# Optimization experiments

Hardware: AMD Instinct MI355X
Metric: run time of the kernel (lower is better)

The kernel has to match this reference:

```python
import jax, jax.numpy as jnp
import numpy as np
import math

SEQ_LEN = 2048
DIM = 4096
N_HEADS = 32
N_KV_HEADS = 8
HEAD_DIM = DIM // N_HEADS  # 128
ROPE_THETA = 500000.0
W_SCALE = 0.02


def _precompute_freqs(head_dim, end, theta=ROPE_THETA):
    freq = 1.0 / theta ** (jnp.arange(0, head_dim, 2, dtype=jnp.float32) / head_dim)  # [hd/2]
    t = jnp.arange(end, dtype=jnp.float32)
    f = t[:, None] * freq[None, :]  # [S, hd/2]
    return jnp.cos(f), jnp.sin(f)


def _apply_rope(x, cos, sin):
    # x: [S, H, hd]; interleaved even/odd rotation, matching torch ::2 / 1::2 indexing
    xe = x[:, :, 0::2]
    xo = x[:, :, 1::2]
    c = cos[:, None, :]  # [S, 1, hd/2]
    s = sin[:, None, :]
    re = xe * c - xo * s
    ro = xe * s + xo * c
    # re-interleave: out[..., 2i] = re[..., i], out[..., 2i+1] = ro[..., i]
    return jnp.stack([re, ro], axis=-1).reshape(x.shape)


def setup_inputs() -> dict:
    key = jax.random.key(0)
    k = jax.random.split(key, 5)
    x = jax.random.normal(k[0], (SEQ_LEN, DIM), dtype=jnp.float32)
    wq = jax.random.normal(k[1], (DIM, DIM), dtype=jnp.float32) * W_SCALE
    wk = jax.random.normal(k[2], (N_KV_HEADS * HEAD_DIM, DIM), dtype=jnp.float32) * W_SCALE
    wv = jax.random.normal(k[3], (N_KV_HEADS * HEAD_DIM, DIM), dtype=jnp.float32) * W_SCALE
    wo = jax.random.normal(k[4], (DIM, DIM), dtype=jnp.float32) * W_SCALE
    return {"x": x, "wq": wq, "wk": wk, "wv": wv, "wo": wo}


def reference(x, wq, wk, wv, wo):
    S = SEQ_LEN
    rep = N_HEADS // N_KV_HEADS  # 4

    Q = (x @ wq.T).reshape(S, N_HEADS, HEAD_DIM)
    K = (x @ wk.T).reshape(S, N_KV_HEADS, HEAD_DIM)
    V = (x @ wv.T).reshape(S, N_KV_HEADS, HEAD_DIM)

    cos, sin = _precompute_freqs(HEAD_DIM, S)
    Q = _apply_rope(Q, cos, sin)
    K = _apply_rope(K, cos, sin)

    # GQA: repeat_interleave(K, rep, dim=1) maps query head h -> kv group h // rep.
    # Express natively with a grouped einsum instead of materializing repeated K/V.
    Qg = Q.transpose(1, 0, 2).reshape(N_KV_HEADS, rep, S, HEAD_DIM)  # [g, r, S, d]
    Kt = K.transpose(1, 0, 2)  # [g, S, d]
    Vt = V.transpose(1, 0, 2)  # [g, S, d]

    scores = jnp.einsum('grqd,gkd->grqk', Qg, Kt) / math.sqrt(HEAD_DIM)
    mask = jnp.triu(jnp.full((S, S), -jnp.inf, dtype=scores.dtype), k=1)
    probs = jax.nn.softmax(scores + mask, axis=-1)
    out = jnp.einsum('grqk,gkd->grqd', probs, Vt)  # [g, r, S, d]

    out = out.reshape(N_HEADS, S, HEAD_DIM).transpose(1, 0, 2).reshape(S, N_HEADS * HEAD_DIM)
    return out @ wo.T
```

## Files before the change

### kernel.cpp

```cpp
#include <hip/hip_runtime.h>

typedef unsigned short u16;
typedef short short8 __attribute__((ext_vector_type(8)));
typedef float f32x4 __attribute__((ext_vector_type(4)));
typedef unsigned short u16x4 __attribute__((ext_vector_type(4)));

typedef short8 short8_a __attribute__((may_alias));
typedef f32x4 f32x4_a __attribute__((may_alias));
typedef u16x4 u16x4_a __attribute__((may_alias));
typedef unsigned int uint_a __attribute__((may_alias));

__device__ __forceinline__ u16 f2b(float f) {
  unsigned u = __float_as_uint(f);
  u += 0x7FFFu + ((u >> 16) & 1u);
  return (u16)(u >> 16);
}

__device__ __forceinline__ void mfma_b(f32x4& d, short8 a, short8 b) {
  asm("v_mfma_f32_16x16x32_bf16 %0, %1, %2, %0" : "+v"(d) : "v"(a), "v"(b));
}

__device__ __forceinline__ void guard4(f32x4& a, f32x4& b, f32x4& c, f32x4& d) {
  asm volatile("s_nop 7\n\ts_nop 7" : "+v"(a), "+v"(b), "+v"(c), "+v"(d));
}
__device__ __forceinline__ void guard8(f32x4* o) {
  asm volatile("s_nop 7\n\ts_nop 7"
               : "+v"(o[0]), "+v"(o[1]), "+v"(o[2]), "+v"(o[3]),
                 "+v"(o[4]), "+v"(o[5]), "+v"(o[6]), "+v"(o[7]));
}

__device__ __forceinline__ void gload16(const void* g, void* l) {
  __builtin_amdgcn_global_load_lds((__attribute__((address_space(1))) void*)(g),
                                   (__attribute__((address_space(3))) void*)(l),
                                   16, 0, 0);
}

__device__ __forceinline__ void bar_v4() {
  asm volatile("s_waitcnt vmcnt(4)\n\ts_barrier" ::: "memory");
}
__device__ __forceinline__ void bar_v0() {
  asm volatile("s_waitcnt vmcnt(0)\n\ts_barrier" ::: "memory");
}

__global__ __launch_bounds__(256)
void k_prep(const float* __restrict__ x, const float* __restrict__ wq,
            const float* __restrict__ wk, const float* __restrict__ wv,
            const float* __restrict__ wo, u16* __restrict__ xb,
            u16* __restrict__ wB, u16* __restrict__ wob,
            float* __restrict__ cost, float* __restrict__ sint) {
  const long i = (long)blockIdx.x * 256 + threadIdx.x;
  const float* src;
  u16* dst;
  long j;
  if (i < 6291456) {
    if (i < 2097152) { src = x; dst = xb; j = i; }
    else { src = wq; dst = wB; j = i - 2097152; }
  } else if (i < 8388608) {
    if (i < 7340032) { src = wk; dst = wB + 16777216; j = i - 6291456; }
    else { src = wv; dst = wB + 20971520; j = i - 7340032; }
  } else if (i < 12582912) {
    src = wo; dst = wob; j = i - 8388608;
  } else {
    long ti = i - 12582912;
    int s = (int)(ti >> 6), jj = (int)(ti & 63);
    float freq = powf(500000.0f, -(float)jj * (1.0f / 64.0f));
    float a = (float)s * freq;
    float sv, cv;
    sincosf(a, &sv, &cv);
    cost[ti] = cv;
    sint[ti] = sv;
    return;
  }
  f32x4 v = ((const f32x4_a*)src)[j];
  u16x4 o;
  o[0] = f2b(v[0]); o[1] = f2b(v[1]); o[2] = f2b(v[2]); o[3] = f2b(v[3]);
  ((u16x4_a*)dst)[j] = o;
}

#define QK_SCALE 0.08838834764831845f
template <int EPI>
__global__ __launch_bounds__(256, 2)
void k_gemm_t(const u16* __restrict__ A, const u16* __restrict__ B,
              float* __restrict__ C, int M, int N, int K,
              const float* __restrict__ cost, const float* __restrict__ sint,
              u16* __restrict__ Qb, u16* __restrict__ Kb, u16* __restrict__ Vt) {
  __shared__ u16 As[12288];
  __shared__ u16 Bs[12288];
  const int tid = threadIdx.x;
  const int w = tid >> 6, lane = tid & 63;
  const int hi = lane >> 4, lo = lane & 15;
  const int nwg = gridDim.x;
  int bid = blockIdx.x;
  if ((nwg & 7) == 0) bid = (bid & 7) * (nwg >> 3) + (bid >> 3);
  const int ntn = N >> 7;
  const int tm = bid / ntn, tn = bid - tm * ntn;
  const int m0 = tm << 7, n0 = tn << 7;
  const int wr = w >> 1, wc = w & 1;

  const int rowl = w * 16 + (lane >> 2);
  const int ks = (((lane & 3) ^ ((lane >> 3) & 3)) << 3);
  const u16* Ag0 = A + (long)(m0 + rowl) * K + ks;
  const u16* Ag1 = A + (long)(m0 + 64 + rowl) * K + ks;
  const u16* Bg0 = B + (long)(n0 + rowl) * K + ks;
  const u16* Bg1 = B + (long)(n0 + 64 + rowl) * K + ks;
  const int sb = w * 512;

  f32x4 acc[4][4] = {};
  const int hs = hi ^ ((lo >> 1) & 3);
  const int aoff = (wr * 64 + lo) * 32 + hs * 8;
  const int boff = (wc * 64 + lo) * 32 + hs * 8;

  const int nt = K >> 5;
  int c0 = 0, c1 = 4096, c2 = 8192;

  gload16(Ag0, As + c0 + sb);       gload16(Ag1, As + c0 + sb + 2048);
  gload16(Bg0, Bs + c0 + sb);       gload16(Bg1, Bs + c0 + sb + 2048);
  gload16(Ag0 + 32, As + c1 + sb);  gload16(Ag1 + 32, As + c1 + sb + 2048);
  gload16(Bg0 + 32, Bs + c1 + sb);  gload16(Bg1 + 32, Bs + c1 + sb + 2048);
  bar_v4();

  for (int t = 0; t < nt; ++t) {
    if (t + 2 < nt) {
      const int k0 = (t + 2) << 5;
      gload16(Ag0 + k0, As + c2 + sb);
      gload16(Ag1 + k0, As + c2 + sb + 2048);
      gload16(Bg0 + k0, Bs + c2 + sb);
      gload16(Bg1 + k0, Bs + c2 + sb + 2048);
    }
    short8 af[4], bf[4];
#pragma unroll
    for (int m = 0; m < 4; ++m)
      af[m] = *(const short8_a*)(As + c0 + aoff + m * 512);
#pragma unroll
    for (int n = 0; n < 4; ++n)
      bf[n] = *(const short8_a*)(Bs + c0 + boff + n * 512);
    __builtin_amdgcn_s_setprio(1);
#pragma unroll
    for (int m = 0; m < 4; ++m)
#pragma unroll
      for (int n = 0; n < 4; ++n) mfma_b(acc[m][n], af[m], bf[n]);
    __builtin_amdgcn_s_setprio(0);
    if (t + 2 < nt) bar_v4();
    else bar_v0();
    const int tmp = c0; c0 = c1; c1 = c2; c2 = tmp;
  }
  guard8(&acc[0][0]);
  guard8(&acc[2][0]);

  if constexpr (EPI == 0) {
#pragma unroll
    for (int m = 0; m < 4; ++m) {
      const int row0 = m0 + wr * 64 + m * 16 + hi * 4;
#pragma unroll
      for (int n = 0; n < 4; ++n) {
        const int col = n0 + wc * 64 + n * 16 + lo;
#pragma unroll
        for (int r = 0; r < 4; ++r)
          C[(long)(row0 + r) * N + col] = acc[m][n][r];
      }
    }
  } else {
    if (n0 < 5120) {
      const bool isQ = (n0 < 4096);
#pragma unroll
      for (int m = 0; m < 4; ++m) {
        const int row0 = m0 + wr * 64 + m * 16 + hi * 4;
#pragma unroll
        for (int n = 0; n < 4; ++n) {
          const int c = n0 + wc * 64 + n * 16 + lo;
          const int j0 = (c & 127) >> 1;
          const bool even = ((c & 1) == 0);
#pragma unroll
          for (int r = 0; r < 4; ++r) {
            float own = acc[m][n][r];
            float part = __shfl_xor(own, 1);
            const int s_ = row0 + r;
            const float cv = cost[s_ * 64 + j0];
            const float sv = sint[s_ * 64 + j0];
            float res = even ? (own * cv - part * sv) : (part * sv + own * cv);
            if (isQ)
              Qb[(long)s_ * 4096 + c] = f2b(res * QK_SCALE);
            else
              Kb[(long)s_ * 1024 + (c - 4096)] = f2b(res);
          }
        }
      }
    } else {
#pragma unroll
      for (int m = 0; m < 4; ++m) {
        const int row0 = m0 + wr * 64 + m * 16 + hi * 4;
#pragma unroll
        for (int n = 0; n < 4; ++n) {
          const int vc = n0 - 5120 + wc * 64 + n * 16 + lo;
          u16x4 pk;
#pragma unroll
          for (int r = 0; r < 4; ++r) pk[r] = f2b(acc[m][n][r]);
          *(u16x4_a*)(Vt + (long)vc * 2048 + row0) = pk;
        }
      }
    }
  }
}

#define KLD 136
#define VLD 72
__global__ __launch_bounds__(256, 2)
void k_attn(const u16* __restrict__ Qb, const u16* __restrict__ Kb,
            const u16* __restrict__ Vt, u16* __restrict__ Ab) {
  __shared__ u16 Ks[64 * KLD];
  __shared__ u16 Vs[128 * VLD];
  __shared__ u16 Ps[4 * 16 * VLD];

  const int tid = threadIdx.x;
  const int w = tid >> 6, lane = tid & 63;
  const int hi = lane >> 4, lo = lane & 15;
  const int qt = 31 - (blockIdx.x >> 5);
  const int h = blockIdx.x & 31;
  const int hkv = h >> 2;
  const int q0 = qt * 64;
  const int qrow = q0 + w * 16 + lo;

  short8 qf[4];
#pragma unroll
  for (int c = 0; c < 4; ++c)
    qf[c] = *(const short8_a*)(Qb + (long)qrow * 4096 + h * 128 + c * 32 + hi * 8);

  f32x4 o[8] = {};
  float m_run = -1e30f, l_run = 0.f;
  u16* Pw = Ps + w * (16 * VLD);

  const int ntiles = qt + 1;
  for (int t = 0; t < ntiles; ++t) {
    const int kv0 = t * 64;
    __syncthreads();
#pragma unroll
    for (int r = 0; r < 4; ++r) {
      int i = r * 256 + tid;
      int key = i >> 4, d8 = (i & 15) * 8;
      short8 v = *(const short8_a*)(Kb + (long)(kv0 + key) * 1024 + hkv * 128 + d8);
      *(short8_a*)(Ks + key * KLD + d8) = v;
    }
#pragma unroll
    for (int r = 0; r < 4; ++r) {
      int i = r * 256 + tid;
      int dd = i >> 3, k8 = (i & 7) * 8;
      short8 v = *(const short8_a*)(Vt + (long)hkv * 262144 + (long)dd * 2048 + kv0 + k8);
      *(short8_a*)(Vs + dd * VLD + k8) = v;
    }
    __syncthreads();

    f32x4 sc[4] = {};
#pragma unroll
    for (int c = 0; c < 4; ++c) {
#pragma unroll
      for (int kt = 0; kt < 4; ++kt) {
        short8 kf = *(const short8_a*)(Ks + (kt * 16 + lo) * KLD + c * 32 + hi * 8);
        mfma_b(sc[kt], kf, qf[c]);
      }
    }
    guard4(sc[0], sc[1], sc[2], sc[3]);

    if (t == ntiles - 1) {
#pragma unroll
      for (int kt = 0; kt < 4; ++kt)
#pragma unroll
        for (int r = 0; r < 4; ++r) {
          int key = kv0 + kt * 16 + hi * 4 + r;
          if (key > qrow) sc[kt][r] = -1e30f;
        }
    }
    float tmax = -1e30f;
#pragma unroll
    for (int kt = 0; kt < 4; ++kt)
#pragma unroll
      for (int r = 0; r < 4; ++r) tmax = fmaxf(tmax, sc[kt][r]);
    tmax = fmaxf(tmax, __shfl_xor(tmax, 16));
    tmax = fmaxf(tmax, __shfl_xor(tmax, 32));
    float m_new = fmaxf(m_run, tmax);
    float scale = __expf(m_run - m_new);
    float psum = 0.f;
    float p[16];
#pragma unroll
    for (int kt = 0; kt < 4; ++kt)
#pragma unroll
      for (int r = 0; r < 4; ++r) {
        float pv = __expf(sc[kt][r] - m_new);
        p[kt * 4 + r] = pv;
        psum += pv;
      }
    psum += __shfl_xor(psum, 16);
    psum += __shfl_xor(psum, 32);
    l_run = l_run * scale + psum;
    m_run = m_new;
    float srow[4];
#pragma unroll
    for (int r = 0; r < 4; ++r) srow[r] = __shfl(scale, hi * 4 + r);
#pragma unroll
    for (int n = 0; n < 8; ++n)
#pragma unroll
      for (int r = 0; r < 4; ++r) o[n][r] *= srow[r];
#pragma unroll
    for (int kt = 0; kt < 4; ++kt) {
      unsigned p01 = (unsigned)f2b(p[kt * 4]) | ((unsigned)f2b(p[kt * 4 + 1]) << 16);
      unsigned p23 = (unsigned)f2b(p[kt * 4 + 2]) | ((unsigned)f2b(p[kt * 4 + 3]) << 16);
      *(uint_a*)(Pw + lo * VLD + kt * 16 + hi * 4) = p01;
      *(uint_a*)(Pw + lo * VLD + kt * 16 + hi * 4 + 2) = p23;
    }
    __syncthreads();
#pragma unroll
    for (int c = 0; c < 2; ++c) {
      short8 pf = *(const short8_a*)(Pw + lo * VLD + c * 32 + hi * 8);
#pragma unroll
      for (int n = 0; n < 8; ++n) {
        short8 vf = *(const short8_a*)(Vs + (n * 16 + lo) * VLD + c * 32 + hi * 8);
        mfma_b(o[n], pf, vf);
      }
    }
  }
  guard8(o);

  float inv = 1.0f / l_run;
  float irow[4];
#pragma unroll
  for (int r = 0; r < 4; ++r) irow[r] = __shfl(inv, hi * 4 + r);
#pragma unroll
  for (int n = 0; n < 8; ++n)
#pragma unroll
    for (int r = 0; r < 4; ++r) {
      int q = q0 + w * 16 + hi * 4 + r;
      Ab[(long)q * 4096 + h * 128 + n * 16 + lo] = f2b(o[n][r] * irow[r]);
    }
}

extern "C" void kernel_launch(void* const* d_in, const int* in_sizes, int n_in,
                              void* d_out, int out_size, void* d_ws, size_t ws_size,
                              hipStream_t stream) {
  const float* x = (const float*)d_in[0];
  const float* wq = (const float*)d_in[1];
  const float* wk = (const float*)d_in[2];
  const float* wv = (const float*)d_in[3];
  const float* wo = (const float*)d_in[4];
  float* out = (float*)d_out;
  char* ws = (char*)d_ws;

  size_t off = 0;
  u16* xb = (u16*)(ws + off); off += 16777216;
  u16* wB = (u16*)(ws + off); off += 50331648;
  u16* wob = (u16*)(ws + off); off += 33554432;
  u16* Qb = (u16*)(ws + off); off += 16777216;
  u16* Kb = (u16*)(ws + off); off += 4194304;
  u16* Vtb = (u16*)(ws + off); off += 4194304;
  float* cost = (float*)(ws + off); off += 524288;
  float* sint = (float*)(ws + off); off += 524288;
  u16* Ab = (u16*)(ws + off); off += 16777216;

  k_prep<<<49664, 256, 0, stream>>>(x, wq, wk, wv, wo, xb, wB, wob, cost, sint);

  k_gemm_t<1><<<768, 256, 0, stream>>>(xb, wB, nullptr, 2048, 6144, 4096,
                                       cost, sint, Qb, Kb, Vtb);

  k_attn<<<1024, 256, 0, stream>>>(Qb, Kb, Vtb, Ab);

  k_gemm_t<0><<<512, 256, 0, stream>>>(Ab, wob, out, 2048, 4096, 4096,
                                       nullptr, nullptr, nullptr, nullptr, nullptr);
}
```

Measured before the change: 378.3 us.

## Use 256x256-tile 512-thread GEMM with double-buffered LDS for QKV projection

Replaces the fused QKV projection GEMM with a new kernel that computes 256x256 output tiles per 8-wave workgroup. It uses 128 KB of dynamic shared memory, double-buffered 64-wide K slices, and interleaves async global-to-LDS loads between the two MFMA halves. The larger tile is meant to raise operand reuse and reduce global/LDS traffic per FLOP, keeping the RoPE/scale/V-transpose epilogue. It launches only 192 workgroups, so fewer than all CUs get work, and occupancy drops to one block per CU.

After: 371.2 us. About the same (-1.9%).

```diff
diff --git a/kernel.cpp b/kernel.cpp
--- a/kernel.cpp
+++ b/kernel.cpp
@@ -35,11 +35,11 @@
                                    16, 0, 0);
 }
 
+__device__ __forceinline__ void bar_v0() {
+  asm volatile("s_waitcnt vmcnt(0)\n\ts_barrier" ::: "memory");
+}
 __device__ __forceinline__ void bar_v4() {
   asm volatile("s_waitcnt vmcnt(4)\n\ts_barrier" ::: "memory");
-}
-__device__ __forceinline__ void bar_v0() {
-  asm volatile("s_waitcnt vmcnt(0)\n\ts_barrier" ::: "memory");
 }
 
 __global__ __launch_bounds__(256)
@@ -78,12 +78,142 @@
 }
 
 #define QK_SCALE 0.08838834764831845f
+__global__ __launch_bounds__(512, 2)
+void k_gemm8(const u16* __restrict__ A, const u16* __restrict__ B,
+             const float* __restrict__ cost, const float* __restrict__ sint,
+             u16* __restrict__ Qb, u16* __restrict__ Kb, u16* __restrict__ Vt) {
+  extern __shared__ u16 lds[];
+  const int K = 4096;
+  const int tid = threadIdx.x;
+  const int w = tid >> 6, lane = tid & 63;
+  const int hi = lane >> 4, lo = lane & 15;
+  const int wr = w >> 2, wc = w & 3;
+  int bid = blockIdx.x;
+  bid = (bid & 7) * 24 + (bid >> 3);
+  const int tm = bid / 24, tn = bid - (bid / 24) * 24;
+  const int m0 = tm << 8, n0 = tn << 8;
+
+  const int kx = (((tid & 7) ^ ((tid >> 3) & 7)) << 3);
+  const int r3 = tid >> 3;
+
+  f32x4 acc[8][4] = {};
+  short8 afr[4][2], bfr[4][2];
+
+  const int sA0 = (wr * 128 + lo) * 64;
+  const int sB0 = (wc * 64 + lo) * 64;
+  const int sl0 = ((0 * 4 + hi) ^ (lo & 7)) * 8;
+  const int sl1 = ((1 * 4 + hi) ^ (lo & 7)) * 8;
+
+#define STAGE_A(sbuf, h, kt)                                                    \
+  {                                                                             \
+    _Pragma("unroll") for (int l = 0; l < 2; ++l) {                             \
+      gload16(A + (long)(m0 + (h)*128 + l * 64 + r3) * K + (kt)*64 + kx,        \
+              lds + (sbuf)*16384 + ((h)*128 + l * 64 + w * 8) * 64);            \
+    }                                                                           \
+  }
+#define STAGE_B(sbuf, h, kt)                                                    \
+  {                                                                             \
+    _Pragma("unroll") for (int l = 0; l < 2; ++l) {                             \
+      gload16(B + (long)(n0 + (h)*128 + l * 64 + r3) * K + (kt)*64 + kx,        \
+              lds + 32768 + (sbuf)*16384 + ((h)*128 + l * 64 + w * 8) * 64);    \
+    }                                                                           \
+  }
+
+  STAGE_A(0, 0, 0); STAGE_A(0, 1, 0);
+  STAGE_B(0, 0, 0); STAGE_B(0, 1, 0);
+  bar_v0();
+
+  const int NI = K >> 7;
+#define HALF_ITER(buf, stile, sbuf, dostage)                                    \
+  {                                                                             \
+    const u16* Ab_ = lds + (buf)*16384;                                         \
+    const u16* Bb_ = lds + 32768 + (buf)*16384;                                 \
+    if (dostage) { STAGE_A(sbuf, 0, stile); STAGE_A(sbuf, 1, stile); }          \
+    _Pragma("unroll") for (int fn = 0; fn < 4; ++fn) {                          \
+      bfr[fn][0] = *(const short8_a*)(Bb_ + sB0 + fn * 1024 + sl0);             \
+      bfr[fn][1] = *(const short8_a*)(Bb_ + sB0 + fn * 1024 + sl1);             \
+    }                                                                           \
+    _Pragma("unroll") for (int fm = 0; fm < 4; ++fm) {                          \
+      afr[fm][0] = *(const short8_a*)(Ab_ + sA0 + fm * 1024 + sl0);             \
+      afr[fm][1] = *(const short8_a*)(Ab_ + sA0 + fm * 1024 + sl1);             \
+    }                                                                           \
+    __builtin_amdgcn_s_setprio(1);                                              \
+    _Pragma("unroll") for (int fm = 0; fm < 4; ++fm)                            \
+      _Pragma("unroll") for (int fn = 0; fn < 4; ++fn) {                        \
+        mfma_b(acc[fm][fn], afr[fm][0], bfr[fn][0]);                            \
+        mfma_b(acc[fm][fn], afr[fm][1], bfr[fn][1]);                            \
+      }                                                                         \
+    __builtin_amdgcn_s_setprio(0);                                              \
+    if (dostage) { STAGE_B(sbuf, 0, stile); STAGE_B(sbuf, 1, stile); }          \
+    _Pragma("unroll") for (int fm = 0; fm < 4; ++fm) {                          \
+      afr[fm][0] = *(const short8_a*)(Ab_ + sA0 + (fm + 4) * 1024 + sl0);       \
+      afr[fm][1] = *(const short8_a*)(Ab_ + sA0 + (fm + 4) * 1024 + sl1);       \
+    }                                                                           \
+    __builtin_amdgcn_s_setprio(1);                                              \
+    _Pragma("unroll") for (int fm = 0; fm < 4; ++fm)                            \
+      _Pragma("unroll") for (int fn = 0; fn < 4; ++fn) {                        \
+        mfma_b(acc[fm + 4][fn], afr[fm][0], bfr[fn][0]);                        \
+        mfma_b(acc[fm + 4][fn], afr[fm][1], bfr[fn][1]);                        \
+      }                                                                         \
+    __builtin_amdgcn_s_setprio(0);                                              \
+    bar_v0();                                                                   \
+  }
+
+  for (int it = 0; it < NI; ++it) {
+    HALF_ITER(0, 2 * it + 1, 1, true);
+    HALF_ITER(1, 2 * it + 2, 0, (it + 1 < NI));
+  }
+
+  guard8(&acc[0][0]); guard8(&acc[2][0]); guard8(&acc[4][0]); guard8(&acc[6][0]);
+
+  if (n0 < 5120) {
+    const bool isQ = (n0 < 4096);
+#pragma unroll
+    for (int fm = 0; fm < 8; ++fm) {
+      const int row0 = m0 + wr * 128 + fm * 16 + hi * 4;
+#pragma unroll
+      for (int fn = 0; fn < 4; ++fn) {
+        const int c = n0 + wc * 64 + fn * 16 + lo;
+        const int j0 = (c & 127) >> 1;
+        const bool even = ((c & 1) == 0);
+#pragma unroll
+        for (int r = 0; r < 4; ++r) {
+          float own = acc[fm][fn][r];
+          float part = __shfl_xor(own, 1);
+          const int s_ = row0 + r;
+          const float cv = cost[s_ * 64 + j0];
+          const float sv = sint[s_ * 64 + j0];
+          float res = even ? (own * cv - part * sv) : (part * sv + own * cv);
+          if (isQ)
+            Qb[(long)s_ * 4096 + c] = f2b(res * QK_SCALE);
+          else
+            Kb[(long)s_ * 1024 + (c - 4096)] = f2b(res);
+        }
+      }
+    }
+  } else {
+#pragma unroll
+    for (int fm = 0; fm < 8; ++fm) {
+      const int row0 = m0 + wr * 128 + fm * 16 + hi * 4;
+#pragma unroll
+      for (int fn = 0; fn < 4; ++fn) {
+        const int vc = n0 - 5120 + wc * 64 + fn * 16 + lo;
+        u16x4 pk;
+#pragma unroll
+        for (int r = 0; r < 4; ++r) pk[r] = f2b(acc[fm][fn][r]);
+        *(u16x4_a*)(Vt + (long)vc * 2048 + row0) = pk;
+      }
+    }
+  }
+#undef HALF_ITER
+#undef STAGE_A
+#undef STAGE_B
+}
+
 template <int EPI>
 __global__ __launch_bounds__(256, 2)
 void k_gemm_t(const u16* __restrict__ A, const u16* __restrict__ B,
-              float* __restrict__ C, int M, int N, int K,
-              const float* __restrict__ cost, const float* __restrict__ sint,
-              u16* __restrict__ Qb, u16* __restrict__ Kb, u16* __restrict__ Vt) {
+              float* __restrict__ C, int M, int N, int K) {
   __shared__ u16 As[12288];
   __shared__ u16 Bs[12288];
   const int tid = threadIdx.x;
@@ -147,57 +277,15 @@
   guard8(&acc[0][0]);
   guard8(&acc[2][0]);
 
-  if constexpr (EPI == 0) {
-#pragma unroll
-    for (int m = 0; m < 4; ++m) {
-      const int row0 = m0 + wr * 64 + m * 16 + hi * 4;
-#pragma unroll
-      for (int n = 0; n < 4; ++n) {
-        const int col = n0 + wc * 64 + n * 16 + lo;
-#pragma unroll
-        for (int r = 0; r < 4; ++r)
-          C[(long)(row0 + r) * N + col] = acc[m][n][r];
-      }
-    }
-  } else {
-    if (n0 < 5120) {
-      const bool isQ = (n0 < 4096);
-#pragma unroll
-      for (int m = 0; m < 4; ++m) {
-        const int row0 = m0 + wr * 64 + m * 16 + hi * 4;
-#pragma unroll
-        for (int n = 0; n < 4; ++n) {
-          const int c = n0 + wc * 64 + n * 16 + lo;
-          const int j0 = (c & 127) >> 1;
-          const bool even = ((c & 1) == 0);
-#pragma unroll
-          for (int r = 0; r < 4; ++r) {
-            float own = acc[m][n][r];
-            float part = __shfl_xor(own, 1);
-            const int s_ = row0 + r;
-            const float cv = cost[s_ * 64 + j0];
-            const float sv = sint[s_ * 64 + j0];
-            float res = even ? (own * cv - part * sv) : (part * sv + own * cv);
-            if (isQ)
-              Qb[(long)s_ * 4096 + c] = f2b(res * QK_SCALE);
-            else
-              Kb[(long)s_ * 1024 + (c - 4096)] = f2b(res);
-          }
-        }
-      }
-    } else {
-#pragma unroll
-      for (int m = 0; m < 4; ++m) {
-        const int row0 = m0 + wr * 64 + m * 16 + hi * 4;
-#pragma unroll
-        for (int n = 0; n < 4; ++n) {
-          const int vc = n0 - 5120 + wc * 64 + n * 16 + lo;
-          u16x4 pk;
-#pragma unroll
-          for (int r = 0; r < 4; ++r) pk[r] = f2b(acc[m][n][r]);
-          *(u16x4_a*)(Vt + (long)vc * 2048 + row0) = pk;
-        }
-      }
+#pragma unroll
+  for (int m = 0; m < 4; ++m) {
+    const int row0 = m0 + wr * 64 + m * 16 + hi * 4;
+#pragma unroll
+    for (int n = 0; n < 4; ++n) {
+      const int col = n0 + wc * 64 + n * 16 + lo;
+#pragma unroll
+      for (int r = 0; r < 4; ++r)
+        C[(long)(row0 + r) * N + col] = acc[m][n][r];
     }
   }
 }
@@ -354,13 +442,18 @@
   float* sint = (float*)(ws + off); off += 524288;
   u16* Ab = (u16*)(ws + off); off += 16777216;
 
+  static bool attr_set = false;
+  if (!attr_set) {
+    hipFuncSetAttribute((const void*)k_gemm8,
+                        hipFuncAttributeMaxDynamicSharedMemorySize, 131072);
+    attr_set = true;
+  }
+
   k_prep<<<49664, 256, 0, stream>>>(x, wq, wk, wv, wo, xb, wB, wob, cost, sint);
 
-  k_gemm_t<1><<<768, 256, 0, stream>>>(xb, wB, nullptr, 2048, 6144, 4096,
-                                       cost, sint, Qb, Kb, Vtb);
+  k_gemm8<<<192, 512, 131072, stream>>>(xb, wB, cost, sint, Qb, Kb, Vtb);
 
   k_attn<<<1024, 256, 0, stream>>>(Qb, Kb, Vtb, Ab);
 
-  k_gemm_t<0><<<512, 256, 0, stream>>>(Ab, wob, out, 2048, 4096, 4096,
-                                       nullptr, nullptr, nullptr, nullptr, nullptr);
-}
+  k_gemm_t<0><<<512, 256, 0, stream>>>(Ab, wob, out, 2048, 4096, 4096);
+}
```
